# Kernel tuning notes

Measured on AMD Instinct MI355X. Metric: run time of the kernel, lower is better.

## Reference

```python
import jax, jax.numpy as jnp
import numpy as np

N = 50000
DIM = 768   # input_dim == feature dim (self.L)
D_ATT = 128 # self.D


def setup_inputs() -> dict:
    key = jax.random.key(0)
    ks = jax.random.split(key, 6)
    s = lambda fan_in: 1.0 / np.sqrt(fan_in)
    return {
        "x": jax.random.normal(ks[0], (1, N, DIM), dtype=jnp.float32),
        "W_feat": jax.random.normal(ks[1], (DIM, DIM), dtype=jnp.float32) * s(DIM),
        "b_feat": jax.random.normal(ks[2], (DIM,), dtype=jnp.float32) * s(DIM),
        "W_a": jax.random.normal(ks[3], (D_ATT, DIM), dtype=jnp.float32) * s(DIM),
        "W_b": jax.random.normal(ks[4], (D_ATT, DIM), dtype=jnp.float32) * s(DIM),
        "W_c": jax.random.normal(ks[5], (1, D_ATT), dtype=jnp.float32) * s(D_ATT),
    }


def reference(x, W_feat, b_feat, W_a, W_b, W_c):
    # x: [1, N, DIM] -> squeeze bag dim -> [N, DIM]
    h = jax.nn.relu(jnp.einsum('nd,ed->ne', x[0], W_feat) + b_feat)  # [N, 768]
    a = jax.nn.relu(jnp.einsum('nd,kd->nk', h, W_a))      # [N, 128]
    b = jax.nn.sigmoid(jnp.einsum('nd,kd->nk', h, W_b))   # [N, 128]
    logits = jnp.einsum('nk,ok->on', a * b, W_c)           # [1, N] (transpose fused)
    A = jax.nn.softmax(logits, axis=-1)                    # [1, N]
    return jnp.einsum('on,nd->od', A, h)                   # [1, 768]
```

## Files before the change

kernel.cpp:

```cpp
#include <hip/hip_runtime.h>
#include <hip/hip_bf16.h>
#include <stdint.h>

#define DEVINL __device__ __forceinline__

using bf16x8 = __attribute__((ext_vector_type(8))) short;
using f32x4  = __attribute__((ext_vector_type(4))) float;

static constexpr int NPTS = 50000;
static constexpr int NPAD = 50048;
static constexpr int DIM  = 768;
static constexpr int DATT = 128;
static constexpr int NRB  = NPAD / 128;

DEVINL ushort f2b(float f) {
  uint32_t u = __float_as_uint(f);
  u += 0x7fffu + ((u >> 16) & 1u);
  return (ushort)(u >> 16);
}
DEVINL float b2f(ushort u) { return __uint_as_float(((uint32_t)u) << 16); }

DEVINL void gload_lds16(const void* g, void* l) {
  __builtin_amdgcn_global_load_lds((const __attribute__((address_space(1))) void*)g,
                                   (__attribute__((address_space(3))) void*)l,
                                   16, 0, 0);
}

__global__ void cvt8_kernel(const float* __restrict__ src, ushort* __restrict__ dst,
                            int n8_src, int n8_dst) {
  const int stride = gridDim.x * blockDim.x;
  for (int i = blockIdx.x * blockDim.x + threadIdx.x; i < n8_dst; i += stride) {
    float4 v0 = {0.f, 0.f, 0.f, 0.f}, v1 = {0.f, 0.f, 0.f, 0.f};
    if (i < n8_src) {
      const float4* s4 = (const float4*)src;
      v0 = s4[(long)i * 2];
      v1 = s4[(long)i * 2 + 1];
    }
    ushort4 o0 = { f2b(v0.x), f2b(v0.y), f2b(v0.z), f2b(v0.w) };
    ushort4 o1 = { f2b(v1.x), f2b(v1.y), f2b(v1.z), f2b(v1.w) };
    ((ushort4*)dst)[(long)i * 2]     = o0;
    ((ushort4*)dst)[(long)i * 2 + 1] = o1;
  }
}

__global__ void cvt_weights_kernel(const float* __restrict__ Wf, const float* __restrict__ Wa,
                                   const float* __restrict__ Wb,
                                   ushort* __restrict__ wfb, ushort* __restrict__ wab,
                                   ushort* __restrict__ wbb) {
  const int NF = DIM * DIM / 8, NA = DATT * DIM / 8;
  int i = blockIdx.x * blockDim.x + threadIdx.x;
  const float* src; ushort* dst; int j;
  if (i < NF)               { src = Wf; dst = wfb; j = i; }
  else if (i < NF + NA)     { src = Wa; dst = wab; j = i - NF; }
  else if (i < NF + 2 * NA) { src = Wb; dst = wbb; j = i - NF - NA; }
  else return;
  const float4* s4 = (const float4*)src;
  float4 v0 = s4[(long)j * 2];
  float4 v1 = s4[(long)j * 2 + 1];
  ushort4 o0 = { f2b(v0.x), f2b(v0.y), f2b(v0.z), f2b(v0.w) };
  ushort4 o1 = { f2b(v1.x), f2b(v1.y), f2b(v1.z), f2b(v1.w) };
  ((ushort4*)dst)[(long)j * 2]     = o0;
  ((ushort4*)dst)[(long)j * 2 + 1] = o1;
}

__global__ __launch_bounds__(512)
void gemm_h_kernel(const ushort* __restrict__ A, const ushort* __restrict__ B,
                   const float* __restrict__ bias, ushort* __restrict__ H) {
  __shared__ ushort As[128 * 64];
  __shared__ ushort Bs[256 * 64];
  const int tid  = threadIdx.x;
  const int wid  = tid >> 6;
  const int lane = tid & 63;

  const int nwg = NRB * 3;
  const int q = nwg >> 3, r = nwg & 7;
  const int xcd = blockIdx.x & 7, idx = blockIdx.x >> 3;
  const int wgid = (xcd < r ? xcd * (q + 1) : r * (q + 1) + (xcd - r) * q) + idx;
  const int row0 = (wgid / 3) * 128;
  const int col0 = (wgid % 3) * 256;

  const int wrow = (wid >> 2) * 64;
  const int wcol = (wid & 3) * 64;

  f32x4 acc[4][4] = {};

  const int ld_r = lane >> 3;
  const int ld_c = (lane & 7) * 8;

  for (int k0 = 0; k0 < DIM; k0 += 64) {
    __syncthreads();
#pragma unroll
    for (int i = 0; i < 2; ++i) {
      const int ch = i * 8 + wid;
      gload_lds16(A + (long)(row0 + ch * 8 + ld_r) * DIM + k0 + ld_c, As + ch * 512);
    }
#pragma unroll
    for (int i = 0; i < 4; ++i) {
      const int ch = i * 8 + wid;
      gload_lds16(B + (long)(col0 + ch * 8 + ld_r) * DIM + k0 + ld_c, Bs + ch * 512);
    }
    __syncthreads();
#pragma unroll
    for (int kk = 0; kk < 2; ++kk) {
      const int kc = kk * 32 + (lane >> 4) * 8;
      bf16x8 a[4];
#pragma unroll
      for (int m = 0; m < 4; ++m)
        a[m] = *(const bf16x8*)(As + (wrow + m * 16 + (lane & 15)) * 64 + kc);
#pragma unroll
      for (int n = 0; n < 4; ++n) {
        bf16x8 b = *(const bf16x8*)(Bs + (wcol + n * 16 + (lane & 15)) * 64 + kc);
#pragma unroll
        for (int m = 0; m < 4; ++m)
          acc[m][n] = __builtin_amdgcn_mfma_f32_16x16x32_bf16(a[m], b, acc[m][n], 0, 0, 0);
      }
    }
  }

  const int lq = lane >> 4;
  const int lc = lane & 15;
#pragma unroll
  for (int n = 0; n < 4; ++n) {
    const int cg = col0 + wcol + n * 16 + lc;
    const float bv = bias[cg];
#pragma unroll
    for (int m = 0; m < 4; ++m) {
      const int rg = row0 + wrow + m * 16 + lq * 4;
#pragma unroll
      for (int r2 = 0; r2 < 4; ++r2) {
        float v = acc[m][n][r2] + bv;
        v = fmaxf(v, 0.0f);
        H[(long)(rg + r2) * DIM + cg] = f2b(v);
      }
    }
  }
}

__global__ __launch_bounds__(512)
void gate_kernel(const ushort* __restrict__ Hm, const ushort* __restrict__ Wa,
                 const ushort* __restrict__ Wb, const float* __restrict__ Wc,
                 float* __restrict__ logits) {
  __shared__ ushort Hs [128 * 64];
  __shared__ ushort Was[128 * 64];
  __shared__ ushort Wbs[128 * 64];
  const int tid  = threadIdx.x;
  const int wid  = tid >> 6;
  const int lane = tid & 63;
  const int row0 = blockIdx.x * 128;

  f32x4 fa[8] = {};
  f32x4 fb[8] = {};

  const int ld_r = lane >> 3;
  const int ld_c = (lane & 7) * 8;

  for (int k0 = 0; k0 < DIM; k0 += 64) {
    __syncthreads();
#pragma unroll
    for (int i = 0; i < 2; ++i) {
      const int ch = i * 8 + wid;
      const int r  = ch * 8 + ld_r;
      gload_lds16(Hm + (long)(row0 + r) * DIM + k0 + ld_c, Hs  + ch * 512);
      gload_lds16(Wa + (long)r * DIM        + k0 + ld_c, Was + ch * 512);
      gload_lds16(Wb + (long)r * DIM        + k0 + ld_c, Wbs + ch * 512);
    }
    __syncthreads();
#pragma unroll
    for (int kk = 0; kk < 2; ++kk) {
      const int kc = kk * 32 + (lane >> 4) * 8;
      bf16x8 h = *(const bf16x8*)(Hs + (wid * 16 + (lane & 15)) * 64 + kc);
#pragma unroll
      for (int n = 0; n < 8; ++n) {
        bf16x8 wa = *(const bf16x8*)(Was + (n * 16 + (lane & 15)) * 64 + kc);
        bf16x8 wb = *(const bf16x8*)(Wbs + (n * 16 + (lane & 15)) * 64 + kc);
        fa[n] = __builtin_amdgcn_mfma_f32_16x16x32_bf16(h, wa, fa[n], 0, 0, 0);
        fb[n] = __builtin_amdgcn_mfma_f32_16x16x32_bf16(h, wb, fb[n], 0, 0, 0);
      }
    }
  }

  const int lc = lane & 15;
  const int lq = lane >> 4;
  float g[4];
#pragma unroll
  for (int r = 0; r < 4; ++r) {
    float s = 0.f;
#pragma unroll
    for (int n = 0; n < 8; ++n) {
      float av = fmaxf(fa[n][r], 0.f);
      float sg = 1.f / (1.f + expf(-fb[n][r]));
      s += av * sg * Wc[n * 16 + lc];
    }
    s += __shfl_xor(s, 1);
    s += __shfl_xor(s, 2);
    s += __shfl_xor(s, 4);
    s += __shfl_xor(s, 8);
    g[r] = s;
  }
  if (lc == 0) {
    const int rbase = row0 + wid * 16 + lq * 4;
#pragma unroll
    for (int r = 0; r < 4; ++r) {
      const int nidx = rbase + r;
      if (nidx < NPTS) logits[nidx] = g[r];
    }
  }
}

__global__ __launch_bounds__(1024)
void softmax_stats_kernel(const float* __restrict__ logits, float* __restrict__ stats) {
  __shared__ float red[1024];
  const int tid = threadIdx.x;
  float m = -1e30f;
  for (int i = tid; i < NPTS; i += 1024) m = fmaxf(m, logits[i]);
  red[tid] = m; __syncthreads();
  for (int s = 512; s > 0; s >>= 1) {
    if (tid < s) red[tid] = fmaxf(red[tid], red[tid + s]);
    __syncthreads();
  }
  m = red[0];
  __syncthreads();
  float sum = 0.f;
  for (int i = tid; i < NPTS; i += 1024) sum += expf(logits[i] - m);
  red[tid] = sum; __syncthreads();
  for (int s = 512; s > 0; s >>= 1) {
    if (tid < s) red[tid] += red[tid + s];
    __syncthreads();
  }
  if (tid == 0) { stats[0] = m; stats[1] = red[0]; }
}

__global__ __launch_bounds__(192)
void weighted_partial_kernel(const ushort* __restrict__ Hm, const float* __restrict__ logits,
                             const float* __restrict__ stats, float* __restrict__ part) {
  __shared__ float w[128];
  const int b = blockIdx.x, tid = threadIdx.x;
  const int n0 = b * 128;
  if (tid < 128) {
    const int n = n0 + tid;
    w[tid] = (n < NPTS) ? expf(logits[n] - stats[0]) : 0.f;
  }
  __syncthreads();
  float4 acc = {0.f, 0.f, 0.f, 0.f};
  const ushort* hp = Hm + (long)n0 * DIM + tid * 4;
#pragma unroll 4
  for (int r = 0; r < 128; ++r) {
    const float wr = w[r];
    ushort4 v = *(const ushort4*)(hp + (long)r * DIM);
    acc.x += wr * b2f(v.x);
    acc.y += wr * b2f(v.y);
    acc.z += wr * b2f(v.z);
    acc.w += wr * b2f(v.w);
  }
  ((float4*)(part + (long)b * DIM))[tid] = acc;
}

__global__ void final_reduce_kernel(const float* __restrict__ part,
                                    const float* __restrict__ stats,
                                    float* __restrict__ out) {
  const int c = blockIdx.x * blockDim.x + threadIdx.x;
  if (c >= DIM) return;
  float s = 0.f;
  for (int b = 0; b < NRB; ++b) s += part[(long)b * DIM + c];
  out[c] = s / stats[1];
}

extern "C" void kernel_launch(void* const* d_in, const int* in_sizes, int n_in,
                              void* d_out, int out_size, void* d_ws, size_t ws_size,
                              hipStream_t stream) {
  const float* x  = (const float*)d_in[0];
  const float* Wf = (const float*)d_in[1];
  const float* bf = (const float*)d_in[2];
  const float* Wa = (const float*)d_in[3];
  const float* Wb = (const float*)d_in[4];
  const float* Wc = (const float*)d_in[5];
  float* out = (float*)d_out;

  char* p = (char*)d_ws;
  ushort* xb  = (ushort*)p; p += (size_t)NPAD * DIM * 2;
  ushort* hb  = (ushort*)p; p += (size_t)NPAD * DIM * 2;
  ushort* wfb = (ushort*)p; p += (size_t)DIM * DIM * 2;
  ushort* wab = (ushort*)p; p += (size_t)DATT * DIM * 2;
  ushort* wbb = (ushort*)p; p += (size_t)DATT * DIM * 2;
  float* logits = (float*)p; p += (size_t)NPAD * 4;
  float* stats  = (float*)p; p += 256;
  float* part   = (float*)p; p += (size_t)NRB * DIM * 4;

  cvt8_kernel<<<2048, 256, 0, stream>>>(x, xb, NPTS * DIM / 8, NPAD * DIM / 8);
  cvt_weights_kernel<<<384, 256, 0, stream>>>(Wf, Wa, Wb, wfb, wab, wbb);

  gemm_h_kernel<<<NRB * 3, 512, 0, stream>>>(xb, wfb, bf, hb);
  gate_kernel<<<NRB, 512, 0, stream>>>(hb, wab, wbb, Wc, logits);
  softmax_stats_kernel<<<1, 1024, 0, stream>>>(logits, stats);
  weighted_partial_kernel<<<NRB, 192, 0, stream>>>(hb, logits, stats, part);
  final_reduce_kernel<<<3, 256, 0, stream>>>(part, stats, out);
}
```

Before: 234.3 us.

## Triple-buffer GEMM LDS loads with XOR swizzle and 256x128 tiles

Rewrites the feature GEMM main loop so global-to-LDS loads run two stages ahead, using a triple-buffered LDS ring, explicit vmcnt waits and raw barriers. The previous version had a full sync around every k-step. The LDS layout is XOR-swizzled to avoid bank conflicts on MFMA operand reads. The tile shape changes to 256x128 with a fixed XCD-aware block mapping, and NPAD grows to 50176 to fit the new tiles. In exchange, LDS use rises to 144KB per block, which limits occupancy, and the hand-written waitcnt counts are fragile.

Measured after the change: 225.7 us. -3.7%, faster.

```diff
diff --git a/kernel.cpp b/kernel.cpp
--- a/kernel.cpp
+++ b/kernel.cpp
@@ -8,7 +8,7 @@
 using f32x4  = __attribute__((ext_vector_type(4))) float;
 
 static constexpr int NPTS = 50000;
-static constexpr int NPAD = 50048;
+static constexpr int NPAD = 50176;
 static constexpr int DIM  = 768;
 static constexpr int DATT = 128;
 static constexpr int NRB  = NPAD / 128;
@@ -66,55 +66,83 @@
 __global__ __launch_bounds__(512)
 void gemm_h_kernel(const ushort* __restrict__ A, const ushort* __restrict__ B,
                    const float* __restrict__ bias, ushort* __restrict__ H) {
-  __shared__ ushort As[128 * 64];
-  __shared__ ushort Bs[256 * 64];
+  __shared__ ushort lds[3][24576];
+
   const int tid  = threadIdx.x;
   const int wid  = tid >> 6;
   const int lane = tid & 63;
 
-  const int nwg = NRB * 3;
-  const int q = nwg >> 3, r = nwg & 7;
-  const int xcd = blockIdx.x & 7, idx = blockIdx.x >> 3;
-  const int wgid = (xcd < r ? xcd * (q + 1) : r * (q + 1) + (xcd - r) * q) + idx;
-  const int row0 = (wgid / 3) * 128;
-  const int col0 = (wgid % 3) * 256;
-
-  const int wrow = (wid >> 2) * 64;
-  const int wcol = (wid & 3) * 64;
-
-  f32x4 acc[4][4] = {};
-
-  const int ld_r = lane >> 3;
-  const int ld_c = (lane & 7) * 8;
-
-  for (int k0 = 0; k0 < DIM; k0 += 64) {
-    __syncthreads();
+  const int bid  = blockIdx.x;
+  const int wgid = (bid & 7) * 147 + (bid >> 3);
+  const int row0 = (wgid / 6) * 256;
+  const int col0 = (wgid % 6) * 128;
+
+  const int wrow = (wid >> 1) * 64;
+  const int wcol = (wid & 1) * 64;
+
+  const int srow = lane >> 3;
+  const int scol = ((lane & 7) ^ (lane >> 3)) * 8;
+
+  const ushort* Abase = A + (long)row0 * DIM;
+  const ushort* Bbase = B + (long)col0 * DIM;
+
+  auto stage = [&](int t, int buf) {
+    const int k0 = t * 64;
+#pragma unroll
+    for (int i = 0; i < 4; ++i) {
+      const int ch = i * 8 + wid;
+      gload_lds16(Abase + (long)(ch * 8 + srow) * DIM + k0 + scol,
+                  &lds[buf][ch * 512]);
+    }
 #pragma unroll
     for (int i = 0; i < 2; ++i) {
       const int ch = i * 8 + wid;
-      gload_lds16(A + (long)(row0 + ch * 8 + ld_r) * DIM + k0 + ld_c, As + ch * 512);
-    }
-#pragma unroll
-    for (int i = 0; i < 4; ++i) {
-      const int ch = i * 8 + wid;
-      gload_lds16(B + (long)(col0 + ch * 8 + ld_r) * DIM + k0 + ld_c, Bs + ch * 512);
-    }
-    __syncthreads();
+      gload_lds16(Bbase + (long)(ch * 8 + srow) * DIM + k0 + scol,
+                  &lds[buf][16384 + ch * 512]);
+    }
+  };
+
+  f32x4 acc[4][4] = {};
+
+  stage(0, 0);
+  stage(1, 1);
+  int c = 0;
+  for (int t = 0; t < 12; ++t) {
+    if (t < 10) {
+      const int nb = (c == 0) ? 2 : c - 1;
+      stage(t + 2, nb);
+      asm volatile("s_waitcnt vmcnt(12)" ::: "memory");
+    } else if (t == 10) {
+      asm volatile("s_waitcnt vmcnt(6)" ::: "memory");
+    } else {
+      asm volatile("s_waitcnt vmcnt(0)" ::: "memory");
+    }
+    __builtin_amdgcn_s_barrier();
+    __builtin_amdgcn_sched_barrier(0);
+
+    const ushort* Ab = &lds[c][0];
+    const ushort* Bb = &lds[c][16384];
 #pragma unroll
     for (int kk = 0; kk < 2; ++kk) {
-      const int kc = kk * 32 + (lane >> 4) * 8;
+      const int j = kk * 4 + (lane >> 4);
       bf16x8 a[4];
 #pragma unroll
-      for (int m = 0; m < 4; ++m)
-        a[m] = *(const bf16x8*)(As + (wrow + m * 16 + (lane & 15)) * 64 + kc);
+      for (int m = 0; m < 4; ++m) {
+        const int ra = wrow + m * 16 + (lane & 15);
+        a[m] = *(const bf16x8*)(Ab + ra * 64 + ((j ^ (ra & 7)) << 3));
+      }
 #pragma unroll
       for (int n = 0; n < 4; ++n) {
-        bf16x8 b = *(const bf16x8*)(Bs + (wcol + n * 16 + (lane & 15)) * 64 + kc);
+        const int rb = wcol + n * 16 + (lane & 15);
+        bf16x8 b = *(const bf16x8*)(Bb + rb * 64 + ((j ^ (rb & 7)) << 3));
 #pragma unroll
         for (int m = 0; m < 4; ++m)
           acc[m][n] = __builtin_amdgcn_mfma_f32_16x16x32_bf16(a[m], b, acc[m][n], 0, 0, 0);
       }
     }
+    __builtin_amdgcn_sched_barrier(0);
+    __builtin_amdgcn_s_barrier();
+    c = (c == 2) ? 0 : c + 1;
   }
 
   const int lq = lane >> 4;
@@ -289,7 +317,7 @@
   cvt8_kernel<<<2048, 256, 0, stream>>>(x, xb, NPTS * DIM / 8, NPAD * DIM / 8);
   cvt_weights_kernel<<<384, 256, 0, stream>>>(Wf, Wa, Wb, wfb, wab, wbb);
 
-  gemm_h_kernel<<<NRB * 3, 512, 0, stream>>>(xb, wfb, bf, hb);
+  gemm_h_kernel<<<196 * 6, 512, 0, stream>>>(xb, wfb, bf, hb);
   gate_kernel<<<NRB, 512, 0, stream>>>(hb, wab, wbb, Wc, logits);
   softmax_stats_kernel<<<1, 1024, 0, stream>>>(logits, stats);
   weighted_partial_kernel<<<NRB, 192, 0, stream>>>(hb, logits, stats, part);
```
